# Optimization experiments

Hardware: AMD Instinct MI355X
Metric: run time of the kernel (lower is better)

Reference implementation:

```python
import jax, jax.numpy as jnp
import numpy as np

NSMP = 8192
NA = 512  # min_in_features
DOUT = 256  # out_features
REALNA = 520  # input.shape[1] - nSmp


def setup_inputs() -> dict:
    key = jax.random.key(0)
    k1, k2 = jax.random.split(key)
    inp = jax.random.uniform(k1, (NSMP, REALNA + NSMP), dtype=jnp.float32)
    weight = jax.random.uniform(k2, (NA, DOUT), dtype=jnp.float32)  # torch.rand init
    return {"input": inp, "weight": weight}


def reference(input, weight):
    nSmp = NSMP
    na = NA
    X = input[:, :na]  # [nSmp, na]
    realna = input.shape[1] - nSmp
    A = input[:, realna - 8:realna + nSmp - 8]  # [nSmp, nSmp]
    A = A + jnp.eye(nSmp, dtype=input.dtype)
    # D = diag(colsum(A)); D_hat = inverse(D)**0.5 == diag(d^{-1/2})
    d = jnp.sum(A, axis=0)
    d_inv_sqrt = jax.lax.rsqrt(d)
    # DAD = D_hat @ A @ D_hat, applied as row/col scaling (exploits diagonal structure)
    DAD = d_inv_sqrt[:, None] * A * d_inv_sqrt[None, :]
    support = X @ weight  # [nSmp, out]
    output = DAD @ support  # [nSmp, out]
    # bias=False in init, so no bias add
    return jnp.concatenate((output, A), axis=1)  # [nSmp, out + nSmp]
```

## Files before the change

### kernel.cpp

```cpp
#include <hip/hip_runtime.h>

#define NSMP 8192
#define INW  8712
#define OUTW 8448
#define AOFF 512
#define DO   256

typedef __attribute__((ext_vector_type(4)))  float f32x4;
typedef __attribute__((ext_vector_type(8)))  short short8;
typedef __attribute__((ext_vector_type(16))) float floatx16;

typedef __attribute__((address_space(1))) const unsigned int* gptr_t;
typedef __attribute__((address_space(3)))       unsigned int* lptr_t;

__device__ __forceinline__ unsigned pk_bf16(float lo, float hi) {
    return (__float_as_uint(lo) >> 16) | (__float_as_uint(hi) & 0xffff0000u);
}

__device__ __forceinline__ void gload_lds16(const void* g, void* l) {
    __builtin_amdgcn_global_load_lds((gptr_t)g, (lptr_t)l, 16, 0, 0);
}

__global__ __launch_bounds__(256) void kcopy(const float* __restrict__ in,
                                             float* __restrict__ out,
                                             float* __restrict__ d,
                                             unsigned short* __restrict__ aP) {
    const int t  = threadIdx.x;
    const int j0 = blockIdx.x * 1024;
    const int i0 = blockIdx.y * 32;
    const int jc = j0 + 4 * t;
    const float*    src = in  + (size_t)i0 * INW  + AOFF + jc;
    float*          dst = out + (size_t)i0 * OUTW + DO   + jc;
    unsigned short* ap  = aP  + (size_t)i0 * NSMP + jc;
    f32x4 cs = {0.f, 0.f, 0.f, 0.f};
#pragma unroll 8
    for (int r = 0; r < 32; ++r) {
        f32x4 v = __builtin_nontemporal_load((const f32x4*)(src + (size_t)r * INW));
        uint2 pb;
        pb.x = pk_bf16(v[0], v[1]);
        pb.y = pk_bf16(v[2], v[3]);
        *(uint2*)(ap + (size_t)r * NSMP) = pb;
        int di = (i0 + r) - j0;
        if ((di >> 2) == t) {
            int s = di & 3;
            v[0] += (s == 0); v[1] += (s == 1); v[2] += (s == 2); v[3] += (s == 3);
        }
        cs += v;
        __builtin_nontemporal_store(v, (f32x4*)(dst + (size_t)r * OUTW));
    }
    atomicAdd(&d[jc + 0], cs[0]);
    atomicAdd(&d[jc + 1], cs[1]);
    atomicAdd(&d[jc + 2], cs[2]);
    atomicAdd(&d[jc + 3], cs[3]);
}

__global__ __launch_bounds__(256) void ksupport(const float* __restrict__ in,
                                                const float* __restrict__ w,
                                                const float* __restrict__ d,
                                                float* __restrict__ dinv,
                                                unsigned short* __restrict__ sP) {
    const int c  = threadIdx.x;
    const int r0 = blockIdx.x * 8;
    const float* X = in + (size_t)r0 * INW;
    float acc[8] = {0.f, 0.f, 0.f, 0.f, 0.f, 0.f, 0.f, 0.f};
#pragma unroll 4
    for (int k = 0; k < 512; ++k) {
        float wv = w[(size_t)k * DO + c];
#pragma unroll
        for (int r = 0; r < 8; ++r)
            acc[r] = fmaf(X[(size_t)r * INW + k], wv, acc[r]);
    }
    union { unsigned short h[8]; uint4 u; } pk;
#pragma unroll
    for (int r = 0; r < 8; ++r) {
        float dv = rsqrtf(d[r0 + r]);
        unsigned ub = __float_as_uint(acc[r] * dv);
        ub += 0x7fffu + ((ub >> 16) & 1u);
        pk.h[r] = (unsigned short)(ub >> 16);
    }
    *(uint4*)(sP + (size_t)(r0 >> 3) * (DO * 8) + (size_t)c * 8) = pk.u;
    if (c < 8) dinv[r0 + c] = rsqrtf(d[r0 + c]);
}

__global__ __launch_bounds__(256, 2) void kmm(const unsigned short* __restrict__ aP,
                                              const unsigned short* __restrict__ sP,
                                              const float* __restrict__ dinv,
                                              float* __restrict__ out) {
    __shared__ __align__(16) unsigned short lA[3][32 * 64];

    const int b  = blockIdx.x;
    const int rg = ((b >> 4) << 3) + (b & 7);
    const int ch = (b >> 3) & 1;
    const int tid = threadIdx.x;
    const int w = tid >> 6, lane = tid & 63;
    const int m = lane & 31, q = lane >> 5;
    const int i0 = rg * 32;
    const int cc = ch * 128 + w * 32 + m;

    const int srow = lane >> 3;
    const int sg   = lane & 7;
    const unsigned short* aSrc = aP + (size_t)(i0 + w * 8 + srow) * NSMP
                                    + 8 * (sg ^ (srow & 7));
    const unsigned short* bB   = sP + (size_t)q * 2048 + (size_t)cc * 8;

    floatx16 acc;
#pragma unroll
    for (int z = 0; z < 16; ++z) acc[z] = 0.f;

    uint4 Ba0, Ba1, Ba2, Ba3, Bb0, Bb1, Bb2, Bb3;

#define STAGE_A(nb, s) gload_lds16(aSrc + (size_t)(s) * 64, &lA[nb][w * 512])
#define LOAD_B(P, s) do {                                              \
        P##0 = *(const uint4*)(bB + (size_t)((s) * 8 + 0) * 2048);     \
        P##1 = *(const uint4*)(bB + (size_t)((s) * 8 + 2) * 2048);     \
        P##2 = *(const uint4*)(bB + (size_t)((s) * 8 + 4) * 2048);     \
        P##3 = *(const uint4*)(bB + (size_t)((s) * 8 + 6) * 2048);     \
    } while (0)
#define MFMA_KS(cur, Breg, ks) do {                                    \
        union { uint4 u; short8 s8; } fb_; fb_.u = Breg;               \
        const short8 af_ = *(const short8*)(                           \
            &lA[cur][m * 64 + ((((ks) * 2 + q) ^ (m & 7)) * 8)]);      \
        acc = __builtin_amdgcn_mfma_f32_32x32x16_bf16(af_, fb_.s8, acc, 0, 0, 0); \
    } while (0)
#define COMPUTE(cur, P) do {                                           \
        MFMA_KS(cur, P##0, 0); MFMA_KS(cur, P##1, 1);                  \
        MFMA_KS(cur, P##2, 2); MFMA_KS(cur, P##3, 3);                  \
    } while (0)

    STAGE_A(0, 0);  LOAD_B(Ba, 0);
    STAGE_A(1, 1);  LOAD_B(Bb, 1);

    int rd = 0, wr = 2;
    for (int s = 0; s < 128; s += 2) {
        asm volatile("s_waitcnt vmcnt(5)" ::: "memory");
        __builtin_amdgcn_s_barrier();
        STAGE_A(wr, (s + 2) & 127);
        __builtin_amdgcn_s_setprio(1);
        COMPUTE(rd, Ba);
        __builtin_amdgcn_s_setprio(0);
        LOAD_B(Ba, (s + 2) & 127);
        rd = (rd == 2) ? 0 : rd + 1;
        wr = (wr == 2) ? 0 : wr + 1;

        asm volatile("s_waitcnt vmcnt(5)" ::: "memory");
        __builtin_amdgcn_s_barrier();
        STAGE_A(wr, (s + 3) & 127);
        __builtin_amdgcn_s_setprio(1);
        COMPUTE(rd, Bb);
        __builtin_amdgcn_s_setprio(0);
        LOAD_B(Bb, (s + 3) & 127);
        rd = (rd == 2) ? 0 : rd + 1;
        wr = (wr == 2) ? 0 : wr + 1;
    }

#undef STAGE_A
#undef LOAD_B
#undef MFMA_KS
#undef COMPUTE

#pragma unroll
    for (int g = 0; g < 4; ++g) {
        const ushort4 s4 = *(const ushort4*)(sP + (size_t)(i0 / 8 + g) * (DO * 8)
                                                + (size_t)cc * 8 + 4 * q);
        unsigned short sv[4] = {s4.x, s4.y, s4.z, s4.w};
#pragma unroll
        for (int rr = 0; rr < 4; ++rr) {
            const int row = i0 + 8 * g + 4 * q + rr;
            const float idt = __uint_as_float(((unsigned)sv[rr]) << 16);
            out[(size_t)row * OUTW + cc] = (acc[g * 4 + rr] + idt) * dinv[row];
        }
    }
}

extern "C" void kernel_launch(void* const* d_in, const int* in_sizes, int n_in,
                              void* d_out, int out_size, void* d_ws, size_t ws_size,
                              hipStream_t stream) {
    (void)in_sizes; (void)n_in; (void)out_size; (void)ws_size;
    const float* in = (const float*)d_in[0];
    const float* w  = (const float*)d_in[1];
    float* out  = (float*)d_out;
    float* d    = (float*)d_ws;
    float* dinv = d + NSMP;
    unsigned short* sP = (unsigned short*)(d + 2 * NSMP);
    unsigned short* aP = sP + (size_t)1024 * DO * 8;

    hipMemsetAsync(d, 0, NSMP * sizeof(float), stream);
    kcopy<<<dim3(8, 256), 256, 0, stream>>>(in, out, d, aP);
    ksupport<<<1024, 256, 0, stream>>>(in, w, d, dinv, sP);
    kmm<<<512, 256, 0, stream>>>(aP, sP, dinv, out);
}
```

Before: 611.6 us.

## Split-K the bf16 MFMA matmul into two halves with a separate reduce kernel

```diff
diff --git a/kernel.cpp b/kernel.cpp
--- a/kernel.cpp
+++ b/kernel.cpp
@@ -82,13 +82,14 @@
     if (c < 8) dinv[r0 + c] = rsqrtf(d[r0 + c]);
 }
 
-__global__ __launch_bounds__(256, 2) void kmm(const unsigned short* __restrict__ aP,
+__global__ __launch_bounds__(256, 4) void kmm(const unsigned short* __restrict__ aP,
                                               const unsigned short* __restrict__ sP,
-                                              const float* __restrict__ dinv,
-                                              float* __restrict__ out) {
+                                              float* __restrict__ P) {
     __shared__ __align__(16) unsigned short lA[3][32 * 64];
 
-    const int b  = blockIdx.x;
+    const int bl = blockIdx.x;
+    const int kh = bl >> 9;
+    const int b  = bl & 511;
     const int rg = ((b >> 4) << 3) + (b & 7);
     const int ch = (b >> 3) & 1;
     const int tid = threadIdx.x;
@@ -96,6 +97,7 @@
     const int m = lane & 31, q = lane >> 5;
     const int i0 = rg * 32;
     const int cc = ch * 128 + w * 32 + m;
+    const int t0 = kh * 64;
 
     const int srow = lane >> 3;
     const int sg   = lane & 7;
@@ -109,12 +111,12 @@
 
     uint4 Ba0, Ba1, Ba2, Ba3, Bb0, Bb1, Bb2, Bb3;
 
-#define STAGE_A(nb, s) gload_lds16(aSrc + (size_t)(s) * 64, &lA[nb][w * 512])
-#define LOAD_B(P, s) do {                                              \
-        P##0 = *(const uint4*)(bB + (size_t)((s) * 8 + 0) * 2048);     \
-        P##1 = *(const uint4*)(bB + (size_t)((s) * 8 + 2) * 2048);     \
-        P##2 = *(const uint4*)(bB + (size_t)((s) * 8 + 4) * 2048);     \
-        P##3 = *(const uint4*)(bB + (size_t)((s) * 8 + 6) * 2048);     \
+#define STAGE_A(nb, t) gload_lds16(aSrc + (size_t)(t) * 64, &lA[nb][w * 512])
+#define LOAD_B(Q, t) do {                                              \
+        Q##0 = *(const uint4*)(bB + (size_t)((t) * 8 + 0) * 2048);     \
+        Q##1 = *(const uint4*)(bB + (size_t)((t) * 8 + 2) * 2048);     \
+        Q##2 = *(const uint4*)(bB + (size_t)((t) * 8 + 4) * 2048);     \
+        Q##3 = *(const uint4*)(bB + (size_t)((t) * 8 + 6) * 2048);     \
     } while (0)
 #define MFMA_KS(cur, Breg, ks) do {                                    \
         union { uint4 u; short8 s8; } fb_; fb_.u = Breg;               \
@@ -122,33 +124,33 @@
             &lA[cur][m * 64 + ((((ks) * 2 + q) ^ (m & 7)) * 8)]);      \
         acc = __builtin_amdgcn_mfma_f32_32x32x16_bf16(af_, fb_.s8, acc, 0, 0, 0); \
     } while (0)
-#define COMPUTE(cur, P) do {                                           \
-        MFMA_KS(cur, P##0, 0); MFMA_KS(cur, P##1, 1);                  \
-        MFMA_KS(cur, P##2, 2); MFMA_KS(cur, P##3, 3);                  \
+#define COMPUTE(cur, Q) do {                                           \
+        MFMA_KS(cur, Q##0, 0); MFMA_KS(cur, Q##1, 1);                  \
+        MFMA_KS(cur, Q##2, 2); MFMA_KS(cur, Q##3, 3);                  \
     } while (0)
 
-    STAGE_A(0, 0);  LOAD_B(Ba, 0);
-    STAGE_A(1, 1);  LOAD_B(Bb, 1);
+    STAGE_A(0, t0);      LOAD_B(Ba, t0);
+    STAGE_A(1, t0 + 1);  LOAD_B(Bb, t0 + 1);
 
     int rd = 0, wr = 2;
-    for (int s = 0; s < 128; s += 2) {
+    for (int s = 0; s < 64; s += 2) {
         asm volatile("s_waitcnt vmcnt(5)" ::: "memory");
         __builtin_amdgcn_s_barrier();
-        STAGE_A(wr, (s + 2) & 127);
+        STAGE_A(wr, t0 + ((s + 2) & 63));
         __builtin_amdgcn_s_setprio(1);
         COMPUTE(rd, Ba);
         __builtin_amdgcn_s_setprio(0);
-        LOAD_B(Ba, (s + 2) & 127);
+        LOAD_B(Ba, t0 + ((s + 2) & 63));
         rd = (rd == 2) ? 0 : rd + 1;
         wr = (wr == 2) ? 0 : wr + 1;
 
         asm volatile("s_waitcnt vmcnt(5)" ::: "memory");
         __builtin_amdgcn_s_barrier();
-        STAGE_A(wr, (s + 3) & 127);
+        STAGE_A(wr, t0 + ((s + 3) & 63));
         __builtin_amdgcn_s_setprio(1);
         COMPUTE(rd, Bb);
         __builtin_amdgcn_s_setprio(0);
-        LOAD_B(Bb, (s + 3) & 127);
+        LOAD_B(Bb, t0 + ((s + 3) & 63));
         rd = (rd == 2) ? 0 : rd + 1;
         wr = (wr == 2) ? 0 : wr + 1;
     }
@@ -158,17 +160,32 @@
 #undef MFMA_KS
 #undef COMPUTE
 
+    float* Pb = P + (size_t)kh * NSMP * DO;
 #pragma unroll
     for (int g = 0; g < 4; ++g) {
-        const ushort4 s4 = *(const ushort4*)(sP + (size_t)(i0 / 8 + g) * (DO * 8)
-                                                + (size_t)cc * 8 + 4 * q);
-        unsigned short sv[4] = {s4.x, s4.y, s4.z, s4.w};
 #pragma unroll
         for (int rr = 0; rr < 4; ++rr) {
             const int row = i0 + 8 * g + 4 * q + rr;
-            const float idt = __uint_as_float(((unsigned)sv[rr]) << 16);
-            out[(size_t)row * OUTW + cc] = (acc[g * 4 + rr] + idt) * dinv[row];
+            Pb[(size_t)row * DO + cc] = acc[g * 4 + rr];
         }
+    }
+}
+
+__global__ __launch_bounds__(256) void kreduce(const float* __restrict__ P,
+                                               const unsigned short* __restrict__ sP,
+                                               const float* __restrict__ dinv,
+                                               float* __restrict__ out) {
+    const int c = threadIdx.x;
+    const int r0 = blockIdx.x * 4;
+#pragma unroll
+    for (int rr = 0; rr < 4; ++rr) {
+        const int row = r0 + rr;
+        const float p0 = P[(size_t)row * DO + c];
+        const float p1 = P[(size_t)(NSMP + row) * DO + c];
+        const unsigned short sv = sP[(size_t)(row >> 3) * (DO * 8)
+                                     + (size_t)c * 8 + (row & 7)];
+        const float idt = __uint_as_float(((unsigned)sv) << 16);
+        out[(size_t)row * OUTW + c] = (p0 + p1 + idt) * dinv[row];
     }
 }
 
@@ -183,9 +200,11 @@
     float* dinv = d + NSMP;
     unsigned short* sP = (unsigned short*)(d + 2 * NSMP);
     unsigned short* aP = sP + (size_t)1024 * DO * 8;
+    float* P = (float*)(aP + (size_t)NSMP * NSMP);
 
     hipMemsetAsync(d, 0, NSMP * sizeof(float), stream);
     kcopy<<<dim3(8, 256), 256, 0, stream>>>(in, out, d, aP);
     ksupport<<<1024, 256, 0, stream>>>(in, w, d, dinv, sP);
-    kmm<<<512, 256, 0, stream>>>(aP, sP, dinv, out);
-}
+    kmm<<<1024, 256, 0, stream>>>(aP, sP, P);
+    kreduce<<<2048, 256, 0, stream>>>(P, sP, dinv, out);
+}
```

New measurement: 611.2 us. Within noise of the previous version (-0.1%).
